# Performance work log

Hardware: AMD Instinct MI355X
Metric: run time of the kernel (lower is better)

The kernel has to match this reference:

```python
import jax, jax.numpy as jnp
import numpy as np
from itertools import product

S0 = 384          # voxel grid size per max_data_size
N0 = 500_000      # active surface voxels
NF_IN, NF = 2, 16
EPS = 1e-4        # scn.BatchNormReLU default eps


def _make_nbr(lin, S, offs):
    # submanifold rulebook: nbr[k, i] = row of active neighbor of site i at offset k, else sentinel N
    N = len(lin)
    x = lin // (S * S); y = (lin // S) % S; z = lin % S
    nbr = np.full((len(offs), N), N, np.int32)
    for k, (dx, dy, dz) in enumerate(offs):
        nx, ny, nz = x + dx, y + dy, z + dz
        valid = (nx >= 0) & (nx < S) & (ny >= 0) & (ny < S) & (nz >= 0) & (nz < S)
        q = (nx * S + ny) * S + nz
        pos = np.minimum(np.searchsorted(lin, q), N - 1)
        nbr[k] = np.where(valid & (lin[pos] == q), pos, N).astype(np.int32)
    return nbr


def _downsample(lin, S):
    # half-resolution active sites, unpool parent map, and 2x2x2 stride-2 conv rulebook
    x = lin // (S * S); y = (lin // S) % S; z = lin % S
    Sh = S // 2
    plin = ((x // 2) * Sh + (y // 2)) * Sh + (z // 2)
    lin_h = np.unique(plin)
    parent = np.searchsorted(lin_h, plin).astype(np.int32)
    xh = lin_h // (Sh * Sh); yh = (lin_h // Sh) % Sh; zh = lin_h % Sh
    N, Nh = len(lin), len(lin_h)
    down = np.full((8, Nh), N, np.int32)
    for k, (ox, oy, oz) in enumerate(product((0, 1), repeat=3)):
        q = ((2 * xh + ox) * S + (2 * yh + oy)) * S + (2 * zh + oz)
        pos = np.minimum(np.searchsorted(lin, q), N - 1)
        down[k] = np.where(lin[pos] == q, pos, N).astype(np.int32)
    return lin_h, parent, down


def setup_inputs() -> dict:
    rng = np.random.default_rng(0)
    cand = rng.integers(0, S0 ** 3, size=int(N0 * 1.1))
    lin0 = np.unique(cand)[:N0]
    assert len(lin0) == N0
    offs27 = list(product((-1, 0, 1), repeat=3))
    nbr0 = _make_nbr(lin0, S0, offs27)
    lin1, parent01, down01 = _downsample(lin0, S0)
    nbr1 = _make_nbr(lin1, S0 // 2, offs27)
    lin2, parent12, down12 = _downsample(lin1, S0 // 2)
    nbr2 = _make_nbr(lin2, S0 // 4, offs27)

    key = jax.random.key(0)
    ks = jax.random.split(key, 16)
    n = lambda k, sh, sc: jax.random.normal(k, sh, jnp.float32) * sc
    return dict(
        feats=n(ks[0], (N0, NF_IN), 1.0),
        w_p1=n(ks[1], (27, NF_IN, NF), 1.0 / np.sqrt(27 * NF_IN)),
        blk_bn1_g=1.0 + n(ks[2], (3, NF), 0.1), blk_bn1_b=n(ks[3], (3, NF), 0.1),
        blk_w1=n(ks[4], (3, 27, NF, NF), 1.0 / np.sqrt(27 * NF)),
        blk_bn2_g=1.0 + n(ks[5], (3, NF), 0.1), blk_bn2_b=n(ks[6], (3, NF), 0.1),
        blk_w2=n(ks[7], (3, 27, NF, NF), 1.0 / np.sqrt(27 * NF)),
        down_bn_g=1.0 + n(ks[8], (2, NF), 0.1), down_bn_b=n(ks[9], (2, NF), 0.1),
        down_w=n(ks[10], (2, 8, NF, NF), 1.0 / np.sqrt(8 * NF)),
        bn3_g=1.0 + n(ks[11], (3 * NF,), 0.1), bn3_b=n(ks[12], (3 * NF,), 0.1),
        w_sdf=n(ks[13], (3 * NF, 1), 1.0 / np.sqrt(3 * NF)),
        b_sdf=jnp.zeros((1,), jnp.float32),
        nbr0=jnp.asarray(nbr0), nbr1=jnp.asarray(nbr1), nbr2=jnp.asarray(nbr2),
        down01=jnp.asarray(down01), down12=jnp.asarray(down12),
        parent01=jnp.asarray(parent01), parent12=jnp.asarray(parent12),
    )


def _sconv(x, nbr, W):
    # rulebook gather-GEMM-accumulate sparse conv.
    # x: [Nin, Cin], nbr: [K, Nout] (index Nin == inactive sentinel), W: [K, Cin, Cout]
    xp = jnp.concatenate([x, jnp.zeros((1, x.shape[1]), x.dtype)], 0)
    acc0 = jnp.zeros((nbr.shape[1], W.shape[2]), x.dtype)
    def step(acc, kw):
        idx, Wk = kw
        return acc + xp[idx] @ Wk, None
    out, _ = jax.lax.scan(step, acc0, (nbr, W))
    return out


def _bnrelu(x, g, b):
    # SCN BatchNorm: batch stats over active sites only
    m = x.mean(0); v = x.var(0)
    return jax.nn.relu((x - m) * jax.lax.rsqrt(v + EPS) * g + b)


def _res_block(x, nbr, g1, b1, w1, g2, b2, w2):
    # pre-activation residual block, identity skip (in == out channels)
    h = _sconv(_bnrelu(x, g1, b1), nbr, w1)
    h = _sconv(_bnrelu(h, g2, b2), nbr, w2)
    return x + h


def reference(feats, w_p1, blk_bn1_g, blk_bn1_b, blk_w1, blk_bn2_g, blk_bn2_b,
              blk_w2, down_bn_g, down_bn_b, down_w, bn3_g, bn3_b, w_sdf, b_sdf,
              nbr0, nbr1, nbr2, down01, down12, parent01, parent12):
    blk = lambda x, nbr, i: _res_block(x, nbr, blk_bn1_g[i], blk_bn1_b[i], blk_w1[i],
                                       blk_bn2_g[i], blk_bn2_b[i], blk_w2[i])
    x = _sconv(feats, nbr0, w_p1)                                    # p1: submanifold conv nf_in->nf
    r0 = blk(x, nbr0, 0)                                             # FCN level 0 block
    y1 = _sconv(_bnrelu(r0, down_bn_g[0], down_bn_b[0]), down01, down_w[0])  # stride-2 conv
    r1 = blk(y1, nbr1, 1)                                            # level 1 block
    z2 = _sconv(_bnrelu(r1, down_bn_g[1], down_bn_b[1]), down12, down_w[1])
    r2 = blk(z2, nbr2, 2)                                            # level 2 block
    j1 = jnp.concatenate([r1, r2[parent12]], axis=-1)                # UnPool + JoinTable -> 2*nf
    j0 = jnp.concatenate([r0, j1[parent01]], axis=-1)                # UnPool + JoinTable -> 3*nf
    h = _bnrelu(j0, bn3_g, bn3_b)                                    # p3
    return h @ w_sdf + b_sdf                                         # sdf linear, [N0, 1]
```

## Files before the change

kernel.cpp:

```cpp
#include <hip/hip_runtime.h>

#define BN_EPS 1e-4f
#define NREP 16

typedef _Float16 f16x8 __attribute__((ext_vector_type(8)));
typedef _Float16 f16x4 __attribute__((ext_vector_type(4)));
typedef _Float16 f16x2 __attribute__((ext_vector_type(2)));
typedef float f32x4 __attribute__((ext_vector_type(4)));

__global__ __launch_bounds__(256) void build_k(
    const int* __restrict__ nbr, int N, int Nin, int ngroups,
    int* __restrict__ gcnt, int* __restrict__ etap, int* __restrict__ eidx)
{
    __shared__ int stg[4][27 * 16];
    __shared__ int stp[4][27];
    const int wave = threadIdx.x >> 6, lane = threadIdx.x & 63;
    const int l15 = lane & 15, q = lane >> 4;

    for (int grp = blockIdx.x * 4 + wave; grp < ngroups; grp += gridDim.x * 4) {
        const int site = grp * 16 + l15;
        int idxs[27];
#pragma unroll
        for (int t = 0; t < 27; ++t) {
            int v = Nin;
            if (lane < 16 && site < N) v = nbr[(size_t)t * N + site];
            idxs[t] = v;
        }
        int cnt = 0;
#pragma unroll
        for (int t = 0; t < 27; ++t) {
            if (__any(idxs[t] < Nin)) {
                if (lane < 16) stg[wave][cnt * 16 + lane] = idxs[t];
                if (lane == 0) stp[wave][cnt] = t;
                ++cnt;
            }
        }
        const int e0 = grp * 27;
        if (lane == 0) gcnt[grp] = cnt;
        for (int e = q; e < cnt; e += 4)
            eidx[(size_t)(e0 + e) * 16 + l15] = stg[wave][e * 16 + l15];
        for (int e = lane; e < cnt; e += 64)
            etap[e0 + e] = stp[wave][e];
    }
}

__global__ __launch_bounds__(256, 4) void conv16c_k(
    const _Float16* __restrict__ A16,
    const int* __restrict__ gcnt,
    const int* __restrict__ etap,
    const int* __restrict__ eidx,
    const _Float16* __restrict__ WT,
    float* __restrict__ out,
    float* __restrict__ stats_out,
    int Nout, int Nin, int addSkip)
{
    __shared__ _Float16 WTs[27 * 2 * 16 * 8];
    __shared__ float TRS[4][16 * 20];
    __shared__ float RED[4][32];

    const int wave = threadIdx.x >> 6, lane = threadIdx.x & 63;
    const int l15 = lane & 15, q = lane >> 4;
    const int h = q & 1, th = q >> 1;
    float* Tr = TRS[wave];

    {
        const float4* s = (const float4*)WT;
        float4* d = (float4*)WTs;
        for (int v = threadIdx.x; v < 27 * 2 * 16; v += 256) d[v] = s[v];
    }
    __syncthreads();

    const int ngroups = (Nout + 15) >> 4;
    const int rr = lane >> 2, cc = (lane & 3) * 4;
    float sj[4] = {0.f, 0.f, 0.f, 0.f}, qj[4] = {0.f, 0.f, 0.f, 0.f};

    for (int grp = blockIdx.x * 4 + wave; grp < ngroups; grp += gridDim.x * 4) {
        const int C = gcnt[grp];
        const int e0 = grp * 27, np = (C + 1) >> 1;
        const int base = grp * 16, srow = base + rr;

        float4 skip = make_float4(0.f, 0.f, 0.f, 0.f);
        if (addSkip && srow < Nout)
            skip = *(const float4*)(out + (size_t)srow * 16 + cc);

        int myidx[14], mytap[14];
#pragma unroll
        for (int pp = 0; pp < 14; ++pp) {
            const int sidx = 2 * pp + th;
            int id = Nin, tp = 0;
            if (sidx < C) {
                id = eidx[(size_t)(e0 + sidx) * 16 + l15];
                tp = etap[e0 + sidx];
            }
            myidx[pp] = id; mytap[pp] = tp;
        }

        f32x4 acc0 = {0.f, 0.f, 0.f, 0.f}, acc1 = {0.f, 0.f, 0.f, 0.f};
#pragma unroll
        for (int pp = 0; pp < 14; ++pp) {
            if (pp < np) {
                const int idx = myidx[pp];
                f16x8 a = {};
                if (idx < Nin)
                    a = *(const f16x8*)(A16 + (size_t)idx * 16 + h * 8);
                const f16x8 b = *(const f16x8*)(WTs + ((mytap[pp] * 2 + h) * 16 + l15) * 8);
                if (pp & 1) acc1 = __builtin_amdgcn_mfma_f32_16x16x32_f16(a, b, acc1, 0, 0, 0);
                else        acc0 = __builtin_amdgcn_mfma_f32_16x16x32_f16(a, b, acc0, 0, 0, 0);
            }
        }

#pragma unroll
        for (int r = 0; r < 4; ++r)
            Tr[(q * 4 + r) * 20 + l15] = acc0[r] + acc1[r];
        float4 v4;
        v4.x = Tr[rr * 20 + cc + 0] + skip.x;
        v4.y = Tr[rr * 20 + cc + 1] + skip.y;
        v4.z = Tr[rr * 20 + cc + 2] + skip.z;
        v4.w = Tr[rr * 20 + cc + 3] + skip.w;
        if (srow < Nout) {
            *(float4*)(out + (size_t)srow * 16 + cc) = v4;
            sj[0] += v4.x; qj[0] += v4.x * v4.x;
            sj[1] += v4.y; qj[1] += v4.y * v4.y;
            sj[2] += v4.z; qj[2] += v4.z * v4.z;
            sj[3] += v4.w; qj[3] += v4.w * v4.w;
        }
    }

    if (stats_out) {
#pragma unroll
        for (int m = 4; m < 64; m <<= 1) {
#pragma unroll
            for (int j = 0; j < 4; ++j) {
                sj[j] += __shfl_xor(sj[j], m);
                qj[j] += __shfl_xor(qj[j], m);
            }
        }
        if (lane < 4) {
#pragma unroll
            for (int j = 0; j < 4; ++j) {
                RED[wave][lane * 4 + j] = sj[j];
                RED[wave][16 + lane * 4 + j] = qj[j];
            }
        }
        __syncthreads();
        if (threadIdx.x < 32) {
            const int t2 = threadIdx.x;
            float* bank = stats_out + (blockIdx.x & (NREP - 1)) * 128;
            atomicAdd(bank + (t2 < 16 ? t2 : 48 + t2),
                      RED[0][t2] + RED[1][t2] + RED[2][t2] + RED[3][t2]);
        }
    }
}

template <int K>
__global__ __launch_bounds__(256, 4) void conv16_k(
    const _Float16* __restrict__ A16, const int* __restrict__ nbr,
    const _Float16* __restrict__ WB, float* __restrict__ out,
    float* __restrict__ stats_out, int Nout, int Nin, int addSkip)
{
    constexpr int PAIRS = (K + 1) / 2;
    const int wave = threadIdx.x >> 6, lane = threadIdx.x & 63;
    const int l15 = lane & 15, q = lane >> 4;
    const int h = q & 1, th = q >> 1;

    f16x8 bfr[PAIRS];
#pragma unroll
    for (int p = 0; p < PAIRS; ++p)
        bfr[p] = *(const f16x8*)(WB + ((size_t)p * 64 + lane) * 8);

    const int ngroups = (Nout + 15) >> 4;
    float s = 0.f, ss = 0.f;

    for (int grp = blockIdx.x * 4 + wave; grp < ngroups; grp += gridDim.x * 4) {
        const int base = grp * 16;
        const int site = min(base + l15, Nout - 1);
        f32x4 acc0 = {0.f, 0.f, 0.f, 0.f}, acc1 = {0.f, 0.f, 0.f, 0.f};
#pragma unroll
        for (int p = 0; p < PAIRS; ++p) {
            const int t = 2 * p + ((2 * p + 1 < K) ? th : 0);
            const int idx = nbr[(size_t)t * Nout + site];
            f16x8 a = {};
            if (idx < Nin)
                a = *(const f16x8*)(A16 + (size_t)idx * 16 + h * 8);
            if (p & 1) acc1 = __builtin_amdgcn_mfma_f32_16x16x32_f16(a, bfr[p], acc1, 0, 0, 0);
            else       acc0 = __builtin_amdgcn_mfma_f32_16x16x32_f16(a, bfr[p], acc0, 0, 0, 0);
        }
#pragma unroll
        for (int r = 0; r < 4; ++r) {
            const int row = base + q * 4 + r;
            float v = acc0[r] + acc1[r];
            if (row < Nout) {
                float* op = out + (size_t)row * 16 + l15;
                if (addSkip) v += *op;
                *op = v;
                s += v; ss += v * v;
            }
        }
    }

    if (stats_out) {
        s  += __shfl_xor(s, 16);  s  += __shfl_xor(s, 32);
        ss += __shfl_xor(ss, 16); ss += __shfl_xor(ss, 32);
        __shared__ float red[4][32];
        if (lane < 16) { red[wave][l15] = s; red[wave][16 + l15] = ss; }
        __syncthreads();
        if (threadIdx.x < 32) {
            const int t2 = threadIdx.x;
            float* bank = stats_out + (blockIdx.x & (NREP - 1)) * 128;
            atomicAdd(bank + (t2 < 16 ? t2 : 48 + t2),
                      red[0][t2] + red[1][t2] + red[2][t2] + red[3][t2]);
        }
    }
}

__global__ __launch_bounds__(256, 4) void convp1_k(
    const _Float16* __restrict__ F16,
    const int* __restrict__ nbr,
    const _Float16* __restrict__ WB,
    float* __restrict__ out, float* __restrict__ stats_out, int N)
{
    const int wave = threadIdx.x >> 6, lane = threadIdx.x & 63;
    const int l15 = lane & 15, q = lane >> 4;

    f16x8 b0 = *(const f16x8*)(WB + (size_t)lane * 8);
    f16x8 b1 = *(const f16x8*)(WB + ((size_t)64 + lane) * 8);

    const int ngroups = (N + 15) >> 4;
    float s = 0.f, ss = 0.f;

    for (int grp = blockIdx.x * 4 + wave; grp < ngroups; grp += gridDim.x * 4) {
        const int base = grp * 16;
        const int site = min(base + l15, N - 1);
        int tid[8];
#pragma unroll
        for (int u = 0; u < 8; ++u) {
            const int t = (u < 4) ? (q * 4 + u) : (16 + q * 4 + (u - 4));
            tid[u] = (t < 27) ? nbr[(size_t)t * N + site] : N;
        }
        f32x4 acc = {0.f, 0.f, 0.f, 0.f};
#pragma unroll
        for (int mf = 0; mf < 2; ++mf) {
            f16x8 a;
#pragma unroll
            for (int jt = 0; jt < 4; ++jt) {
                const int idx = tid[mf * 4 + jt];
                f16x2 f = {};
                if (idx < N) f = *(const f16x2*)(F16 + (size_t)idx * 2);
                a[jt * 2] = f.x; a[jt * 2 + 1] = f.y;
            }
            acc = __builtin_amdgcn_mfma_f32_16x16x32_f16(a, mf ? b1 : b0, acc, 0, 0, 0);
        }
#pragma unroll
        for (int r = 0; r < 4; ++r) {
            const int row = base + q * 4 + r;
            const float v = acc[r];
            if (row < N) {
                out[(size_t)row * 16 + l15] = v;
                s += v; ss += v * v;
            }
        }
    }

    s  += __shfl_xor(s, 16);  s  += __shfl_xor(s, 32);
    ss += __shfl_xor(ss, 16); ss += __shfl_xor(ss, 32);
    __shared__ float red[4][32];
    if (lane < 16) { red[wave][l15] = s; red[wave][16 + l15] = ss; }
    __syncthreads();
    if (threadIdx.x < 32) {
        const int t2 = threadIdx.x;
        float* bank = stats_out + (blockIdx.x & (NREP - 1)) * 128;
        atomicAdd(bank + (t2 < 16 ? t2 : 48 + t2),
                  red[0][t2] + red[1][t2] + red[2][t2] + red[3][t2]);
    }
}

__global__ void pack_k(const float* __restrict__ w_p1, const float* __restrict__ w1,
                       const float* __restrict__ w2, const float* __restrict__ dw,
                       _Float16* __restrict__ WBp1, _Float16* __restrict__ WT27,
                       _Float16* __restrict__ WB8)
{
    const int b = blockIdx.x;
    if (b == 0) {
        for (int v = threadIdx.x; v < 2 * 64 * 8; v += 256) {
            const int mf = v >> 9, lane = (v >> 3) & 63, j = v & 7;
            const int qq = lane >> 4, n = lane & 15;
            const int kg = mf * 32 + qq * 8 + j;
            const int t = kg >> 1, cin = kg & 1;
            WBp1[v] = (t < 27) ? (_Float16)w_p1[t * 32 + cin * 16 + n] : (_Float16)0.f;
        }
    } else if (b <= 6) {
        const int ti = b - 1, lvl = ti >> 1;
        const float* src = ((ti & 1) ? w2 : w1) + lvl * 6912;
        _Float16* dst = WT27 + (size_t)ti * 6912;
        for (int v = threadIdx.x; v < 6912; v += 256) {
            const int j = v & 7, n = (v >> 3) & 15, hh = (v >> 7) & 1, t = v >> 8;
            dst[v] = (_Float16)src[t * 256 + (hh * 8 + j) * 16 + n];
        }
    } else {
        const int ti = b - 7;
        const float* src = dw + ti * 2048;
        _Float16* dst = WB8 + (size_t)ti * (4 * 64 * 8);
        for (int v = threadIdx.x; v < 4 * 64 * 8; v += 256) {
            const int p = v >> 9, lane = (v >> 3) & 63, j = v & 7;
            const int qq = lane >> 4, n = lane & 15;
            const int t = 2 * p + (qq >> 1);
            const int cin = (qq & 1) * 8 + j;
            dst[v] = (_Float16)src[t * 256 + cin * 16 + n];
        }
    }
}

__global__ __launch_bounds__(256) void apply16_k(
    const float* __restrict__ x, const float* __restrict__ sb,
    _Float16* __restrict__ A16, int N)
{
    const int t = blockIdx.x * 256 + threadIdx.x;
    if (t >= (N + 1) * 4) return;
    const int n = t >> 2, c = (t & 3) * 4;
    f16x4 r;
    if (n == N) {
        r[0] = r[1] = r[2] = r[3] = (_Float16)0.f;
    } else {
        const float4 v = *(const float4*)(x + (size_t)n * 16 + c);
        float vv[4] = {v.x, v.y, v.z, v.w};
#pragma unroll
        for (int i = 0; i < 4; ++i)
            r[i] = (_Float16)fmaxf(fmaf(vv[i], sb[c + i], sb[64 + c + i]), 0.f);
    }
    *(f16x4*)(A16 + (size_t)n * 16 + c) = r;
}

__global__ void f16cvt_k(const float* __restrict__ f, _Float16* __restrict__ F16, int N)
{
    const int t = blockIdx.x * 256 + threadIdx.x;
    if (t > N) return;
    f16x2 r;
    if (t == N) { r[0] = r[1] = (_Float16)0.f; }
    else { const float2 v = *(const float2*)(f + (size_t)t * 2); r[0] = (_Float16)v.x; r[1] = (_Float16)v.y; }
    *(f16x2*)(F16 + (size_t)t * 2) = r;
}

__global__ void fin_k(float* __restrict__ stats, const float* __restrict__ g,
                      const float* __restrict__ b, float* __restrict__ sb,
                      int C, float invN)
{
    const int c = threadIdx.x;
    if (c < C) {
        float su = 0.f, sq = 0.f;
#pragma unroll
        for (int rep = 0; rep < NREP; ++rep) {
            su += stats[rep * 128 + c];
            sq += stats[rep * 128 + 64 + c];
        }
        const float mean = su * invN;
        const float var = sq * invN - mean * mean;
        const float s = g[c] * rsqrtf(var + BN_EPS);
        sb[c] = s;
        sb[64 + c] = fmaf(-mean, s, b[c]);
    }
}

__device__ __forceinline__ float wred(float v) {
#pragma unroll
    for (int off = 32; off > 0; off >>= 1) v += __shfl_xor(v, off);
    return v;
}

__global__ __launch_bounds__(256) void gstats_k(
    const float* __restrict__ R0, const float* __restrict__ R1,
    const float* __restrict__ R2, const int* __restrict__ p01,
    const int* __restrict__ p12, float* __restrict__ stats, int N0)
{
    float s[48], q[48];
#pragma unroll
    for (int c = 0; c < 48; ++c) { s[c] = 0.f; q[c] = 0.f; }

    for (int n = blockIdx.x * blockDim.x + threadIdx.x; n < N0;
         n += gridDim.x * blockDim.x) {
        const int i1 = p01[n];
        const int i2 = p12[i1];
        const float4* a0 = (const float4*)(R0 + (size_t)n * 16);
        const float4* a1 = (const float4*)(R1 + (size_t)i1 * 16);
        const float4* a2 = (const float4*)(R2 + (size_t)i2 * 16);
#pragma unroll
        for (int j = 0; j < 4; ++j) {
            const float4 v = a0[j]; const int c = 4 * j;
            s[c] += v.x; q[c] += v.x * v.x; s[c+1] += v.y; q[c+1] += v.y * v.y;
            s[c+2] += v.z; q[c+2] += v.z * v.z; s[c+3] += v.w; q[c+3] += v.w * v.w;
        }
#pragma unroll
        for (int j = 0; j < 4; ++j) {
            const float4 v = a1[j]; const int c = 16 + 4 * j;
            s[c] += v.x; q[c] += v.x * v.x; s[c+1] += v.y; q[c+1] += v.y * v.y;
            s[c+2] += v.z; q[c+2] += v.z * v.z; s[c+3] += v.w; q[c+3] += v.w * v.w;
        }
#pragma unroll
        for (int j = 0; j < 4; ++j) {
            const float4 v = a2[j]; const int c = 32 + 4 * j;
            s[c] += v.x; q[c] += v.x * v.x; s[c+1] += v.y; q[c+1] += v.y * v.y;
            s[c+2] += v.z; q[c+2] += v.z * v.z; s[c+3] += v.w; q[c+3] += v.w * v.w;
        }
    }

    __shared__ float red[4][96];
    const int wave = threadIdx.x >> 6, lane = threadIdx.x & 63;
#pragma unroll
    for (int c = 0; c < 48; ++c) {
        const float ss = wred(s[c]);
        const float qq = wred(q[c]);
        if (lane == 0) { red[wave][c] = ss; red[wave][48 + c] = qq; }
    }
    __syncthreads();
    const int t = threadIdx.x;
    if (t < 96) {
        float* bank = stats + (blockIdx.x & (NREP - 1)) * 128;
        const float v = red[0][t] + red[1][t] + red[2][t] + red[3][t];
        atomicAdd(bank + (t < 48 ? t : 64 + (t - 48)), v);
    }
}

__global__ __launch_bounds__(256) void out_k(
    const float* __restrict__ R0, const float* __restrict__ R1,
    const float* __restrict__ R2, const int* __restrict__ p01,
    const int* __restrict__ p12, const float* __restrict__ sb,
    const float* __restrict__ wsdf, const float* __restrict__ bsdf,
    float* __restrict__ out, int N0)
{
    const int n = blockIdx.x * 256 + threadIdx.x;
    if (n >= N0) return;
    const int i1 = p01[n];
    const int i2 = p12[i1];
    float acc = bsdf[0];
    const float4* a0 = (const float4*)(R0 + (size_t)n * 16);
    const float4* a1 = (const float4*)(R1 + (size_t)i1 * 16);
    const float4* a2 = (const float4*)(R2 + (size_t)i2 * 16);
#pragma unroll
    for (int j = 0; j < 4; ++j) {
        const float4 v = a0[j]; const int c = 4 * j;
        acc += fmaxf(fmaf(v.x, sb[c+0], sb[64+c+0]), 0.f) * wsdf[c+0];
        acc += fmaxf(fmaf(v.y, sb[c+1], sb[64+c+1]), 0.f) * wsdf[c+1];
        acc += fmaxf(fmaf(v.z, sb[c+2], sb[64+c+2]), 0.f) * wsdf[c+2];
        acc += fmaxf(fmaf(v.w, sb[c+3], sb[64+c+3]), 0.f) * wsdf[c+3];
    }
#pragma unroll
    for (int j = 0; j < 4; ++j) {
        const float4 v = a1[j]; const int c = 16 + 4 * j;
        acc += fmaxf(fmaf(v.x, sb[c+0], sb[64+c+0]), 0.f) * wsdf[c+0];
        acc += fmaxf(fmaf(v.y, sb[c+1], sb[64+c+1]), 0.f) * wsdf[c+1];
        acc += fmaxf(fmaf(v.z, sb[c+2], sb[64+c+2]), 0.f) * wsdf[c+2];
        acc += fmaxf(fmaf(v.w, sb[c+3], sb[64+c+3]), 0.f) * wsdf[c+3];
    }
#pragma unroll
    for (int j = 0; j < 4; ++j) {
        const float4 v = a2[j]; const int c = 32 + 4 * j;
        acc += fmaxf(fmaf(v.x, sb[c+0], sb[64+c+0]), 0.f) * wsdf[c+0];
        acc += fmaxf(fmaf(v.y, sb[c+1], sb[64+c+1]), 0.f) * wsdf[c+1];
        acc += fmaxf(fmaf(v.z, sb[c+2], sb[64+c+2]), 0.f) * wsdf[c+2];
        acc += fmaxf(fmaf(v.w, sb[c+3], sb[64+c+3]), 0.f) * wsdf[c+3];
    }
    out[n] = acc;
}

extern "C" void kernel_launch(void* const* d_in, const int* in_sizes, int n_in,
                              void* d_out, int out_size, void* d_ws, size_t ws_size,
                              hipStream_t stream)
{
    const float* feats = (const float*)d_in[0];
    const float* w_p1  = (const float*)d_in[1];
    const float* bn1g  = (const float*)d_in[2];
    const float* bn1b  = (const float*)d_in[3];
    const float* w1    = (const float*)d_in[4];
    const float* bn2g  = (const float*)d_in[5];
    const float* bn2b  = (const float*)d_in[6];
    const float* w2    = (const float*)d_in[7];
    const float* dbng  = (const float*)d_in[8];
    const float* dbnb  = (const float*)d_in[9];
    const float* dw    = (const float*)d_in[10];
    const float* bn3g  = (const float*)d_in[11];
    const float* bn3b  = (const float*)d_in[12];
    const float* wsdf  = (const float*)d_in[13];
    const float* bsdf  = (const float*)d_in[14];
    const int* nbr0    = (const int*)d_in[15];
    const int* nbr1    = (const int*)d_in[16];
    const int* nbr2    = (const int*)d_in[17];
    const int* down01  = (const int*)d_in[18];
    const int* down12  = (const int*)d_in[19];
    const int* p01     = (const int*)d_in[20];
    const int* p12     = (const int*)d_in[21];

    const int N0 = in_sizes[0] / 2;
    const int N1 = in_sizes[18] / 8;
    const int N2 = in_sizes[19] / 8;
    const int ng0 = (N0 + 15) / 16, ng1 = (N1 + 15) / 16, ng2 = (N2 + 15) / 16;
    const int maxe = ng0 * 27;

    char* wp = (char*)d_ws;
    auto alloc = [&](size_t bytes) { char* r = wp; wp += (bytes + 255) & ~(size_t)255; return r; };
    float* T  = (float*)alloc((size_t)N0 * 16 * 4);
    float* R0 = (float*)alloc((size_t)N0 * 16 * 4);
    float* R1 = (float*)alloc((size_t)N1 * 16 * 4);
    float* R2 = (float*)alloc((size_t)N2 * 16 * 4);
    float* st = (float*)alloc(9 * NREP * 128 * 4);
    float* sb = (float*)alloc(128 * 4);
    _Float16* A16  = (_Float16*)alloc((size_t)(N0 + 1) * 16 * 2);
    _Float16* F16  = (_Float16*)alloc((size_t)(N0 + 1) * 2 * 2);
    _Float16* WBp1 = (_Float16*)alloc(2 * 64 * 8 * 2);
    _Float16* WT27 = (_Float16*)alloc(6 * 6912 * 2);
    _Float16* WB8  = (_Float16*)alloc(2 * 4 * 64 * 8 * 2);
    int* gcnt = (int*)alloc((size_t)ng0 * 4);
    int* etap = (int*)alloc((size_t)maxe * 4);
    int* eidx = (int*)alloc((size_t)maxe * 16 * 4);

    hipMemsetAsync(st, 0, 9 * NREP * 128 * sizeof(float), stream);

    const dim3 B(256);
    auto cgrid = [](int n) {
        const int g = (((n + 15) / 16) + 3) / 4;
        return dim3((unsigned)(g < 2048 ? g : 2048));
    };
    auto agrid = [](int n) { return dim3((unsigned)(((n + 1) * 4 + 255) / 256)); };
    auto lgrid = [](int n) { return dim3((unsigned)((n + 255) / 256)); };
    const float i0 = 1.0f / N0, i1 = 1.0f / N1, i2 = 1.0f / N2;
    auto S = [&](int i) { return st + i * NREP * 128; };
    auto WT = [&](int i) { return WT27 + (size_t)i * 6912; };
    auto W8 = [&](int i) { return WB8 + (size_t)i * (4 * 64 * 8); };

    pack_k<<<9, B, 0, stream>>>(w_p1, w1, w2, dw, WBp1, WT27, WB8);
    f16cvt_k<<<lgrid(N0 + 1), B, 0, stream>>>(feats, F16, N0);

    build_k<<<cgrid(N0), B, 0, stream>>>(nbr0, N0, N0, ng0, gcnt, etap, eidx);
    convp1_k<<<cgrid(N0), B, 0, stream>>>(F16, nbr0, WBp1, R0, S(0), N0);
    fin_k<<<1, 64, 0, stream>>>(S(0), bn1g, bn1b, sb, 16, i0);
    apply16_k<<<agrid(N0), B, 0, stream>>>(R0, sb, A16, N0);
    conv16c_k<<<cgrid(N0), B, 0, stream>>>(A16, gcnt, etap, eidx, WT(0), T, S(1), N0, N0, 0);
    fin_k<<<1, 64, 0, stream>>>(S(1), bn2g, bn2b, sb, 16, i0);
    apply16_k<<<agrid(N0), B, 0, stream>>>(T, sb, A16, N0);
    conv16c_k<<<cgrid(N0), B, 0, stream>>>(A16, gcnt, etap, eidx, WT(1), R0, S(2), N0, N0, 1);
    fin_k<<<1, 64, 0, stream>>>(S(2), dbng, dbnb, sb, 16, i0);
    apply16_k<<<agrid(N0), B, 0, stream>>>(R0, sb, A16, N0);
    conv16_k<8><<<cgrid(N1), B, 0, stream>>>(A16, down01, W8(0), R1, S(3), N1, N0, 0);

    build_k<<<cgrid(N1), B, 0, stream>>>(nbr1, N1, N1, ng1, gcnt, etap, eidx);
    fin_k<<<1, 64, 0, stream>>>(S(3), bn1g + 16, bn1b + 16, sb, 16, i1);
    apply16_k<<<agrid(N1), B, 0, stream>>>(R1, sb, A16, N1);
    conv16c_k<<<cgrid(N1), B, 0, stream>>>(A16, gcnt, etap, eidx, WT(2), T, S(4), N1, N1, 0);
    fin_k<<<1, 64, 0, stream>>>(S(4), bn2g + 16, bn2b + 16, sb, 16, i1);
    apply16_k<<<agrid(N1), B, 0, stream>>>(T, sb, A16, N1);
    conv16c_k<<<cgrid(N1), B, 0, stream>>>(A16, gcnt, etap, eidx, WT(3), R1, S(5), N1, N1, 1);
    fin_k<<<1, 64, 0, stream>>>(S(5), dbng + 16, dbnb + 16, sb, 16, i1);
    apply16_k<<<agrid(N1), B, 0, stream>>>(R1, sb, A16, N1);
    conv16_k<8><<<cgrid(N2), B, 0, stream>>>(A16, down12, W8(1), R2, S(6), N2, N1, 0);

    build_k<<<cgrid(N2), B, 0, stream>>>(nbr2, N2, N2, ng2, gcnt, etap, eidx);
    fin_k<<<1, 64, 0, stream>>>(S(6), bn1g + 32, bn1b + 32, sb, 16, i2);
    apply16_k<<<agrid(N2), B, 0, stream>>>(R2, sb, A16, N2);
    conv16c_k<<<cgrid(N2), B, 0, stream>>>(A16, gcnt, etap, eidx, WT(4), T, S(7), N2, N2, 0);
    fin_k<<<1, 64, 0, stream>>>(S(7), bn2g + 32, bn2b + 32, sb, 16, i2);
    apply16_k<<<agrid(N2), B, 0, stream>>>(T, sb, A16, N2);
    conv16c_k<<<cgrid(N2), B, 0, stream>>>(A16, gcnt, etap, eidx, WT(5), R2, nullptr, N2, N2, 1);

    gstats_k<<<512, B, 0, stream>>>(R0, R1, R2, p01, p12, S(8), N0);
    fin_k<<<1, 64, 0, stream>>>(S(8), bn3g, bn3b, sb, 48, i0);
    out_k<<<lgrid(N0), B, 0, stream>>>(R0, R1, R2, p01, p12, sb, wsdf, bsdf,
                                       (float*)d_out, N0);
}
```

Measured before the change: 748.9 us.

## Pack rulebook index and tap into one word and prefetch next group's entries

The rulebook build now packs each neighbor index and its tap id into a single int, computes active taps with one ballot per four taps instead of 27 sequential any() votes, and writes entries directly without shared-memory staging. The 16-channel submanifold conv reads one combined array instead of separate index and tap arrays, and software-pipelines the loop so the next group's count and 14 entries are loaded while the current group's MFMAs run. This is meant to hide rulebook load latency and cut build cost. In exchange it uses more registers (pe and ce arrays), loads all 14 slots unconditionally (hence the padded allocation), and limits indices to 20 bits.

```diff
diff --git a/kernel.cpp b/kernel.cpp
--- a/kernel.cpp
+++ b/kernel.cpp
@@ -10,45 +10,46 @@
 
 __global__ __launch_bounds__(256) void build_k(
     const int* __restrict__ nbr, int N, int Nin, int ngroups,
-    int* __restrict__ gcnt, int* __restrict__ etap, int* __restrict__ eidx)
-{
-    __shared__ int stg[4][27 * 16];
-    __shared__ int stp[4][27];
+    int* __restrict__ gcnt, int* __restrict__ ent)
+{
     const int wave = threadIdx.x >> 6, lane = threadIdx.x & 63;
     const int l15 = lane & 15, q = lane >> 4;
 
     for (int grp = blockIdx.x * 4 + wave; grp < ngroups; grp += gridDim.x * 4) {
         const int site = grp * 16 + l15;
-        int idxs[27];
-#pragma unroll
-        for (int t = 0; t < 27; ++t) {
-            int v = Nin;
-            if (lane < 16 && site < N) v = nbr[(size_t)t * N + site];
-            idxs[t] = v;
-        }
-        int cnt = 0;
-#pragma unroll
-        for (int t = 0; t < 27; ++t) {
-            if (__any(idxs[t] < Nin)) {
-                if (lane < 16) stg[wave][cnt * 16 + lane] = idxs[t];
-                if (lane == 0) stp[wave][cnt] = t;
-                ++cnt;
-            }
-        }
+        int v[7];
+        unsigned act = 0;
+#pragma unroll
+        for (int p = 0; p < 7; ++p) {
+            const int t = 4 * p + q;
+            int idx = Nin;
+            if (t < 27 && site < N) idx = nbr[(size_t)t * N + site];
+            v[p] = idx;
+            const unsigned long long bal = __ballot(idx < Nin);
+#pragma unroll
+            for (int qq = 0; qq < 4; ++qq) {
+                const int tt = 4 * p + qq;
+                if (tt < 27 && ((bal >> (16 * qq)) & 0xFFFFull)) act |= 1u << tt;
+            }
+        }
+        const int cnt = __popc(act);
+        if (lane == 0) gcnt[grp] = cnt;
         const int e0 = grp * 27;
-        if (lane == 0) gcnt[grp] = cnt;
-        for (int e = q; e < cnt; e += 4)
-            eidx[(size_t)(e0 + e) * 16 + l15] = stg[wave][e * 16 + l15];
-        for (int e = lane; e < cnt; e += 64)
-            etap[e0 + e] = stp[wave][e];
+#pragma unroll
+        for (int p = 0; p < 7; ++p) {
+            const int t = 4 * p + q;
+            if (t < 27 && ((act >> t) & 1)) {
+                const int e = __popc(act & ((1u << t) - 1));
+                ent[(size_t)(e0 + e) * 16 + l15] = (v[p] & 0xFFFFF) | (t << 20);
+            }
+        }
     }
 }
 
 __global__ __launch_bounds__(256, 4) void conv16c_k(
     const _Float16* __restrict__ A16,
     const int* __restrict__ gcnt,
-    const int* __restrict__ etap,
-    const int* __restrict__ eidx,
+    const int* __restrict__ ent,
     const _Float16* __restrict__ WT,
     float* __restrict__ out,
     float* __restrict__ stats_out,
@@ -71,39 +72,54 @@
     __syncthreads();
 
     const int ngroups = (Nout + 15) >> 4;
+    const int stride = gridDim.x * 4;
     const int rr = lane >> 2, cc = (lane & 3) * 4;
     float sj[4] = {0.f, 0.f, 0.f, 0.f}, qj[4] = {0.f, 0.f, 0.f, 0.f};
 
-    for (int grp = blockIdx.x * 4 + wave; grp < ngroups; grp += gridDim.x * 4) {
-        const int C = gcnt[grp];
-        const int e0 = grp * 27, np = (C + 1) >> 1;
+    int grp = blockIdx.x * 4 + wave;
+    int pc = 0, pe[14];
+    if (grp < ngroups) {
+        pc = gcnt[grp];
+        const int e0 = grp * 27;
+#pragma unroll
+        for (int pp = 0; pp < 14; ++pp)
+            pe[pp] = ent[(size_t)(e0 + 2 * pp + th) * 16 + l15];
+    }
+
+    while (grp < ngroups) {
+        const int C = pc;
+        int ce[14];
+#pragma unroll
+        for (int pp = 0; pp < 14; ++pp) ce[pp] = pe[pp];
+
         const int base = grp * 16, srow = base + rr;
-
         float4 skip = make_float4(0.f, 0.f, 0.f, 0.f);
         if (addSkip && srow < Nout)
             skip = *(const float4*)(out + (size_t)srow * 16 + cc);
 
-        int myidx[14], mytap[14];
-#pragma unroll
-        for (int pp = 0; pp < 14; ++pp) {
-            const int sidx = 2 * pp + th;
-            int id = Nin, tp = 0;
-            if (sidx < C) {
-                id = eidx[(size_t)(e0 + sidx) * 16 + l15];
-                tp = etap[e0 + sidx];
-            }
-            myidx[pp] = id; mytap[pp] = tp;
-        }
-
+        const int gn = grp + stride;
+        if (gn < ngroups) {
+            pc = gcnt[gn];
+            const int e0n = gn * 27;
+#pragma unroll
+            for (int pp = 0; pp < 14; ++pp)
+                pe[pp] = ent[(size_t)(e0n + 2 * pp + th) * 16 + l15];
+        }
+
+        const int np = (C + 1) >> 1;
         f32x4 acc0 = {0.f, 0.f, 0.f, 0.f}, acc1 = {0.f, 0.f, 0.f, 0.f};
 #pragma unroll
         for (int pp = 0; pp < 14; ++pp) {
             if (pp < np) {
-                const int idx = myidx[pp];
+                const int sidx = 2 * pp + th;
+                const bool val = sidx < C;
+                const int raw = ce[pp];
+                const int idx = val ? (raw & 0xFFFFF) : Nin;
+                const int tap = val ? ((raw >> 20) & 31) : 0;
                 f16x8 a = {};
                 if (idx < Nin)
                     a = *(const f16x8*)(A16 + (size_t)idx * 16 + h * 8);
-                const f16x8 b = *(const f16x8*)(WTs + ((mytap[pp] * 2 + h) * 16 + l15) * 8);
+                const f16x8 b = *(const f16x8*)(WTs + ((tap * 2 + h) * 16 + l15) * 8);
                 if (pp & 1) acc1 = __builtin_amdgcn_mfma_f32_16x16x32_f16(a, b, acc1, 0, 0, 0);
                 else        acc0 = __builtin_amdgcn_mfma_f32_16x16x32_f16(a, b, acc0, 0, 0, 0);
             }
@@ -124,6 +140,7 @@
             sj[2] += v4.z; qj[2] += v4.z * v4.z;
             sj[3] += v4.w; qj[3] += v4.w * v4.w;
         }
+        grp = gn;
     }
 
     if (stats_out) {
@@ -492,7 +509,7 @@
     const int N1 = in_sizes[18] / 8;
     const int N2 = in_sizes[19] / 8;
     const int ng0 = (N0 + 15) / 16, ng1 = (N1 + 15) / 16, ng2 = (N2 + 15) / 16;
-    const int maxe = ng0 * 27;
+    const int maxe = ng0 * 27 + 64;
 
     char* wp = (char*)d_ws;
     auto alloc = [&](size_t bytes) { char* r = wp; wp += (bytes + 255) & ~(size_t)255; return r; };
@@ -508,8 +525,7 @@
     _Float16* WT27 = (_Float16*)alloc(6 * 6912 * 2);
     _Float16* WB8  = (_Float16*)alloc(2 * 4 * 64 * 8 * 2);
     int* gcnt = (int*)alloc((size_t)ng0 * 4);
-    int* etap = (int*)alloc((size_t)maxe * 4);
-    int* eidx = (int*)alloc((size_t)maxe * 16 * 4);
+    int* ent  = (int*)alloc((size_t)maxe * 16 * 4);
 
     hipMemsetAsync(st, 0, 9 * NREP * 128 * sizeof(float), stream);
 
@@ -528,36 +544,36 @@
     pack_k<<<9, B, 0, stream>>>(w_p1, w1, w2, dw, WBp1, WT27, WB8);
     f16cvt_k<<<lgrid(N0 + 1), B, 0, stream>>>(feats, F16, N0);
 
-    build_k<<<cgrid(N0), B, 0, stream>>>(nbr0, N0, N0, ng0, gcnt, etap, eidx);
+    build_k<<<cgrid(N0), B, 0, stream>>>(nbr0, N0, N0, ng0, gcnt, ent);
     convp1_k<<<cgrid(N0), B, 0, stream>>>(F16, nbr0, WBp1, R0, S(0), N0);
     fin_k<<<1, 64, 0, stream>>>(S(0), bn1g, bn1b, sb, 16, i0);
     apply16_k<<<agrid(N0), B, 0, stream>>>(R0, sb, A16, N0);
-    conv16c_k<<<cgrid(N0), B, 0, stream>>>(A16, gcnt, etap, eidx, WT(0), T, S(1), N0, N0, 0);
+    conv16c_k<<<cgrid(N0), B, 0, stream>>>(A16, gcnt, ent, WT(0), T, S(1), N0, N0, 0);
     fin_k<<<1, 64, 0, stream>>>(S(1), bn2g, bn2b, sb, 16, i0);
     apply16_k<<<agrid(N0), B, 0, stream>>>(T, sb, A16, N0);
-    conv16c_k<<<cgrid(N0), B, 0, stream>>>(A16, gcnt, etap, eidx, WT(1), R0, S(2), N0, N0, 1);
+    conv16c_k<<<cgrid(N0), B, 0, stream>>>(A16, gcnt, ent, WT(1), R0, S(2), N0, N0, 1);
     fin_k<<<1, 64, 0, stream>>>(S(2), dbng, dbnb, sb, 16, i0);
     apply16_k<<<agrid(N0), B, 0, stream>>>(R0, sb, A16, N0);
     conv16_k<8><<<cgrid(N1), B, 0, stream>>>(A16, down01, W8(0), R1, S(3), N1, N0, 0);
 
-    build_k<<<cgrid(N1), B, 0, stream>>>(nbr1, N1, N1, ng1, gcnt, etap, eidx);
+    build_k<<<cgrid(N1), B, 0, stream>>>(nbr1, N1, N1, ng1, gcnt, ent);
     fin_k<<<1, 64, 0, stream>>>(S(3), bn1g + 16, bn1b + 16, sb, 16, i1);
     apply16_k<<<agrid(N1), B, 0, stream>>>(R1, sb, A16, N1);
-    conv16c_k<<<cgrid(N1), B, 0, stream>>>(A16, gcnt, etap, eidx, WT(2), T, S(4), N1, N1, 0);
+    conv16c_k<<<cgrid(N1), B, 0, stream>>>(A16, gcnt, ent, WT(2), T, S(4), N1, N1, 0);
     fin_k<<<1, 64, 0, stream>>>(S(4), bn2g + 16, bn2b + 16, sb, 16, i1);
     apply16_k<<<agrid(N1), B, 0, stream>>>(T, sb, A16, N1);
-    conv16c_k<<<cgrid(N1), B, 0, stream>>>(A16, gcnt, etap, eidx, WT(3), R1, S(5), N1, N1, 1);
+    conv16c_k<<<cgrid(N1), B, 0, stream>>>(A16, gcnt, ent, WT(3), R1, S(5), N1, N1, 1);
     fin_k<<<1, 64, 0, stream>>>(S(5), dbng + 16, dbnb + 16, sb, 16, i1);
     apply16_k<<<agrid(N1), B, 0, stream>>>(R1, sb, A16, N1);
     conv16_k<8><<<cgrid(N2), B, 0, stream>>>(A16, down12, W8(1), R2, S(6), N2, N1, 0);
 
-    build_k<<<cgrid(N2), B, 0, stream>>>(nbr2, N2, N2, ng2, gcnt, etap, eidx);
+    build_k<<<cgrid(N2), B, 0, stream>>>(nbr2, N2, N2, ng2, gcnt, ent);
     fin_k<<<1, 64, 0, stream>>>(S(6), bn1g + 32, bn1b + 32, sb, 16, i2);
     apply16_k<<<agrid(N2), B, 0, stream>>>(R2, sb, A16, N2);
-    conv16c_k<<<cgrid(N2), B, 0, stream>>>(A16, gcnt, etap, eidx, WT(4), T, S(7), N2, N2, 0);
+    conv16c_k<<<cgrid(N2), B, 0, stream>>>(A16, gcnt, ent, WT(4), T, S(7), N2, N2, 0);
     fin_k<<<1, 64, 0, stream>>>(S(7), bn2g + 32, bn2b + 32, sb, 16, i2);
     apply16_k<<<agrid(N2), B, 0, stream>>>(T, sb, A16, N2);
-    conv16c_k<<<cgrid(N2), B, 0, stream>>>(A16, gcnt, etap, eidx, WT(5), R2, nullptr, N2, N2, 1);
+    conv16c_k<<<cgrid(N2), B, 0, stream>>>(A16, gcnt, ent, WT(5), R2, nullptr, N2, N2, 1);
 
     gstats_k<<<512, B, 0, stream>>>(R0, R1, R2, p01, p12, S(8), N0);
     fin_k<<<1, 64, 0, stream>>>(S(8), bn3g, bn3b, sb, 48, i0);
```

Measured after the change: 667.3 us. 1.12x faster.
